# Kernel tuning notes

Hardware: AMD Instinct MI355X
Metric: run time of the kernel (lower is better)

Reference implementation:

```python
import jax, jax.numpy as jnp
import numpy as np

B = 1024
H = 2048  # hidden_size
D = 2048  # input_size

def setup_inputs() -> dict:
    key = jax.random.key(0)
    k1, k2, k3, k4 = jax.random.split(key, 4)
    x = jax.random.normal(k1, (B, D), dtype=jnp.float32)
    h = jax.random.normal(k2, (B, H), dtype=jnp.float32)
    c = jax.random.normal(k3, (B, H), dtype=jnp.float32)
    W = jax.random.normal(k4, (D + H, 4 * H), dtype=jnp.float32) * 0.02
    return {"x": x, "h": h, "c": c, "W": W}

def reference(x, h, c, W):
    # merged = cat([x, h], dim=1); weighted = merged @ W
    merged = jnp.concatenate([x, h], axis=1)          # (B, D+H)
    weighted = merged @ W                             # (B, 4H)
    hid = W.shape[1] // 4
    c_f, c_i, c_g, c_o = jnp.split(weighted, 4, axis=1)
    c_new = c * jax.nn.sigmoid(c_f) + jax.nn.sigmoid(c_i) * jnp.tanh(c_g)
    h_new = jax.nn.sigmoid(c_o) * jnp.tanh(c_new)
    return h_new
```

## Files before the change

kernel.cpp:

```cpp
#include <hip/hip_runtime.h>

typedef __attribute__((ext_vector_type(4))) float          f32x4;
typedef __attribute__((ext_vector_type(8))) __bf16         bf16x8;
typedef __attribute__((ext_vector_type(8))) unsigned short u16x8;

#define B_  1024
#define D_  2048
#define H_  2048
#define K_  4096
#define N_  8192

__device__ __forceinline__ unsigned short f2bf_rne(float f) {
  unsigned u = __builtin_bit_cast(unsigned, f);
  u += 0x7fffu + ((u >> 16) & 1u);
  return (unsigned short)(u >> 16);
}

__device__ __forceinline__ float sigf(float x) {
  return 1.f / (1.f + __expf(-x));
}
__device__ __forceinline__ float tanhf_(float x) {
  float ax = fabsf(x);
  float t  = __expf(-2.f * ax);
  float r  = (1.f - t) / (1.f + t);
  return (x < 0.f) ? -r : r;
}

typedef const __attribute__((address_space(1))) unsigned int* gptr_t;
typedef __attribute__((address_space(3))) unsigned int*       lptr_t;
__device__ __forceinline__ void gl_lds16(const void* g, void* l) {
  __builtin_amdgcn_global_load_lds((gptr_t)g, (lptr_t)l, 16, 0, 0);
}

__global__ __launch_bounds__(256) void k_convert_merged(
    const float* __restrict__ x, const float* __restrict__ h,
    unsigned short* __restrict__ merged) {
  int tid = blockIdx.x * 256 + threadIdx.x;
  int e0  = tid * 8;
  int b   = e0 >> 12;
  int col = e0 & 4095;
  const float* src = (col < D_) ? (x + (size_t)b * D_ + col)
                                : (h + (size_t)b * H_ + (col - D_));
  f32x4 v0 = *(const f32x4*)src;
  f32x4 v1 = *(const f32x4*)(src + 4);
  u16x8 o;
  o[0] = f2bf_rne(v0[0]); o[1] = f2bf_rne(v0[1]);
  o[2] = f2bf_rne(v0[2]); o[3] = f2bf_rne(v0[3]);
  o[4] = f2bf_rne(v1[0]); o[5] = f2bf_rne(v1[1]);
  o[6] = f2bf_rne(v1[2]); o[7] = f2bf_rne(v1[3]);
  *(u16x8*)(merged + e0) = o;
}

__global__ __launch_bounds__(256) void k_transpose_w(
    const float* __restrict__ W, unsigned short* __restrict__ Wt) {
  __shared__ float lt[64 * 64];
  char* lbase = (char*)lt;
  const int t   = threadIdx.x;
  const int g   = blockIdx.x & 3;
  const int jb  = blockIdx.x >> 2;
  const int n0s = g * 2048 + jb * 64;
  const int k0  = blockIdx.y * 64;
#pragma unroll
  for (int i = 0; i < 4; ++i) {
    int kk = (t >> 4) + i * 16;
    int nn = (t & 15) * 4;
    f32x4 v = *(const f32x4*)&W[(size_t)(k0 + kk) * N_ + n0s + nn];
    int by = (kk * 256 + nn * 4) ^ (((kk >> 3) & 7) << 4);
    *(f32x4*)(lbase + by) = v;
  }
  __syncthreads();
#pragma unroll
  for (int i = 0; i < 2; ++i) {
    int jl = (t >> 3) + i * 32;
    int kc = (t & 7) * 8;
    u16x8 o;
#pragma unroll
    for (int jj = 0; jj < 8; ++jj) {
      int k  = kc + jj;
      int by = (k * 256 + jl * 4) ^ (((k >> 3) & 7) << 4);
      o[jj] = f2bf_rne(*(const float*)(lbase + by));
    }
    int nrow = 4 * (jb * 64 + jl) + g;
    *(u16x8*)&Wt[(size_t)nrow * K_ + k0 + kc] = o;
  }
}

#define TM 128
#define TN 128
#define TK 64

__global__ __launch_bounds__(256) void k_gemm(
    const unsigned short* __restrict__ A,
    const unsigned short* __restrict__ Bt,
    const float* __restrict__ c,
    float* __restrict__ out) {
  __shared__ unsigned short As[TM * TK];
  __shared__ unsigned short Bs[TN * TK];
  const int t    = threadIdx.x;
  const int bx   = blockIdx.x;
  const int by   = blockIdx.y;
  const int wid  = t >> 6;
  const int lane = t & 63;
  const int wr   = wid >> 1, wc = wid & 1;
  const int ln15 = lane & 15, kq = lane >> 4;

  const int srow  = t >> 3;
  const int scolb = (t & 7) * 16;

  const char* gA = (const char*)A + (size_t)(by * TM + srow) * (K_ * 2) + scolb;
  const char* gB = (const char*)Bt + (size_t)(bx * TN + srow) * (K_ * 2) + scolb;
  char* lA = (char*)As + srow * (TK * 2) + scolb;
  char* lB = (char*)Bs + srow * (TK * 2) + scolb;

  f32x4 acc[4][4] = {};

  for (int kt = 0; kt < K_ / TK; ++kt) {
    const int gofs = kt * (TK * 2);
#pragma unroll
    for (int i = 0; i < 4; ++i) {
      gl_lds16(gA + (size_t)(i * 32) * (K_ * 2) + gofs, lA + i * 32 * (TK * 2));
      gl_lds16(gB + (size_t)(i * 32) * (K_ * 2) + gofs, lB + i * 32 * (TK * 2));
    }
    __syncthreads();
#pragma unroll
    for (int ks = 0; ks < 2; ++ks) {
      bf16x8 a[4], b[4];
#pragma unroll
      for (int mi = 0; mi < 4; ++mi)
        a[mi] = *(const bf16x8*)((const char*)As +
                 (wr * 64 + mi * 16 + ln15) * (TK * 2) + ks * 64 + kq * 16);
#pragma unroll
      for (int ni = 0; ni < 4; ++ni)
        b[ni] = *(const bf16x8*)((const char*)Bs +
                 (wc * 64 + ni * 16 + ln15) * (TK * 2) + ks * 64 + kq * 16);
#pragma unroll
      for (int mi = 0; mi < 4; ++mi)
#pragma unroll
        for (int ni = 0; ni < 4; ++ni)
          acc[mi][ni] = __builtin_amdgcn_mfma_f32_16x16x32_bf16(
              a[mi], b[ni], acc[mi][ni], 0, 0, 0);
    }
    __syncthreads();
  }

  const int crow0 = by * TM + wr * 64 + kq * 4;
  const int s     = ln15 & 3;
  const int q     = ln15 >> 2;
  const int jbase = bx * 32 + wc * 16 + q;
#pragma unroll
  for (int mi = 0; mi < 4; ++mi)
#pragma unroll
    for (int ni = 0; ni < 4; ++ni)
#pragma unroll
      for (int r = 0; r < 4; ++r) {
        float v  = acc[mi][ni][r];
        float v1 = __shfl_xor(v, 1);
        float v2 = __shfl_xor(v, 2);
        float v3 = __shfl_xor(v, 3);
        if (s == 0) {
          int row = crow0 + mi * 16 + r;
          int j   = jbase + ni * 4;
          float cv = c[(size_t)row * H_ + j];
          float cn = cv * sigf(v) + sigf(v1) * tanhf_(v2);
          out[(size_t)row * H_ + j] = sigf(v3) * tanhf_(cn);
        }
      }
}

extern "C" void kernel_launch(void* const* d_in, const int* in_sizes, int n_in,
                              void* d_out, int out_size, void* d_ws, size_t ws_size,
                              hipStream_t stream) {
  (void)in_sizes; (void)n_in; (void)out_size; (void)ws_size;
  const float* x = (const float*)d_in[0];
  const float* h = (const float*)d_in[1];
  const float* c = (const float*)d_in[2];
  const float* W = (const float*)d_in[3];
  float* out = (float*)d_out;

  char* ws = (char*)d_ws;
  unsigned short* merged = (unsigned short*)ws;
  unsigned short* Wt     = (unsigned short*)(ws + (size_t)8  * 1024 * 1024);

  k_convert_merged<<<2048, 256, 0, stream>>>(x, h, merged);
  k_transpose_w<<<dim3(128, 64), 256, 0, stream>>>(W, Wt);
  k_gemm<<<dim3(N_ / TN, B_ / TM), 256, 0, stream>>>(merged, Wt, c, out);
}
```

Measured before the change: 343.0 us.

## Interleave gate columns in 16-wide groups and use 8 waves per GEMM block

The transposed weight layout now groups the four gates in 16-column chunks rather than interleaving them per column. Each lane therefore holds all four gate values for its column in registers, and the epilogue no longer needs cross-lane shuffles or idle lanes. The GEMM block grows to 512 threads (8 waves), each computing a 32x64 sub-tile with half the accumulators. LDS loads become one contiguous 16-byte chunk per thread in two halves. The aim is to cut epilogue overhead and raise occupancy, at the cost of more waves contending for the same LDS tile and barriers.

Result: faster. 319.8 us (-6.7%).

```diff
diff --git a/kernel.cpp b/kernel.cpp
--- a/kernel.cpp
+++ b/kernel.cpp
@@ -80,7 +80,8 @@
       int by = (k * 256 + jl * 4) ^ (((k >> 3) & 7) << 4);
       o[jj] = f2bf_rne(*(const float*)(lbase + by));
     }
-    int nrow = 4 * (jb * 64 + jl) + g;
+    int j    = jb * 64 + jl;
+    int nrow = ((j >> 4) * 64) + g * 16 + (j & 15);
     *(u16x8*)&Wt[(size_t)nrow * K_ + k0 + kc] = o;
   }
 }
@@ -89,7 +90,7 @@
 #define TN 128
 #define TK 64
 
-__global__ __launch_bounds__(256) void k_gemm(
+__global__ __launch_bounds__(512, 4) void k_gemm(
     const unsigned short* __restrict__ A,
     const unsigned short* __restrict__ Bt,
     const float* __restrict__ c,
@@ -99,42 +100,42 @@
   const int t    = threadIdx.x;
   const int bx   = blockIdx.x;
   const int by   = blockIdx.y;
-  const int wid  = t >> 6;
+  const int w    = t >> 6;
   const int lane = t & 63;
-  const int wr   = wid >> 1, wc = wid & 1;
+  const int wr   = w >> 1, wc = w & 1;
   const int ln15 = lane & 15, kq = lane >> 4;
 
-  const int srow  = t >> 3;
-  const int scolb = (t & 7) * 16;
+  const int srow  = w * 8 + (lane >> 3);
+  const int chunk = (lane & 7) * 16;
 
-  const char* gA = (const char*)A + (size_t)(by * TM + srow) * (K_ * 2) + scolb;
-  const char* gB = (const char*)Bt + (size_t)(bx * TN + srow) * (K_ * 2) + scolb;
-  char* lA = (char*)As + srow * (TK * 2) + scolb;
-  char* lB = (char*)Bs + srow * (TK * 2) + scolb;
+  const char* gA = (const char*)A  + (size_t)(by * TM + srow) * (K_ * 2) + chunk;
+  const char* gB = (const char*)Bt + (size_t)(bx * TN + srow) * (K_ * 2) + chunk;
+  char* lA = (char*)As + t * 16;
+  char* lB = (char*)Bs + t * 16;
+  const size_t half = (size_t)64 * (K_ * 2);
 
-  f32x4 acc[4][4] = {};
+  f32x4 acc[2][4] = {};
 
   for (int kt = 0; kt < K_ / TK; ++kt) {
     const int gofs = kt * (TK * 2);
-#pragma unroll
-    for (int i = 0; i < 4; ++i) {
-      gl_lds16(gA + (size_t)(i * 32) * (K_ * 2) + gofs, lA + i * 32 * (TK * 2));
-      gl_lds16(gB + (size_t)(i * 32) * (K_ * 2) + gofs, lB + i * 32 * (TK * 2));
-    }
+    gl_lds16(gA + gofs,        lA);
+    gl_lds16(gA + half + gofs, lA + 8192);
+    gl_lds16(gB + gofs,        lB);
+    gl_lds16(gB + half + gofs, lB + 8192);
     __syncthreads();
 #pragma unroll
     for (int ks = 0; ks < 2; ++ks) {
-      bf16x8 a[4], b[4];
+      bf16x8 a[2], b[4];
 #pragma unroll
-      for (int mi = 0; mi < 4; ++mi)
+      for (int mi = 0; mi < 2; ++mi)
         a[mi] = *(const bf16x8*)((const char*)As +
-                 (wr * 64 + mi * 16 + ln15) * (TK * 2) + ks * 64 + kq * 16);
+                 (wr * 32 + mi * 16 + ln15) * (TK * 2) + ks * 64 + kq * 16);
 #pragma unroll
       for (int ni = 0; ni < 4; ++ni)
         b[ni] = *(const bf16x8*)((const char*)Bs +
                  (wc * 64 + ni * 16 + ln15) * (TK * 2) + ks * 64 + kq * 16);
 #pragma unroll
-      for (int mi = 0; mi < 4; ++mi)
+      for (int mi = 0; mi < 2; ++mi)
 #pragma unroll
         for (int ni = 0; ni < 4; ++ni)
           acc[mi][ni] = __builtin_amdgcn_mfma_f32_16x16x32_bf16(
@@ -143,28 +144,21 @@
     __syncthreads();
   }
 
-  const int crow0 = by * TM + wr * 64 + kq * 4;
-  const int s     = ln15 & 3;
-  const int q     = ln15 >> 2;
-  const int jbase = bx * 32 + wc * 16 + q;
+  const int row0 = by * TM + wr * 32 + kq * 4;
+  const int j    = (bx * 2 + wc) * 16 + ln15;
 #pragma unroll
-  for (int mi = 0; mi < 4; ++mi)
+  for (int mi = 0; mi < 2; ++mi)
 #pragma unroll
-    for (int ni = 0; ni < 4; ++ni)
-#pragma unroll
-      for (int r = 0; r < 4; ++r) {
-        float v  = acc[mi][ni][r];
-        float v1 = __shfl_xor(v, 1);
-        float v2 = __shfl_xor(v, 2);
-        float v3 = __shfl_xor(v, 3);
-        if (s == 0) {
-          int row = crow0 + mi * 16 + r;
-          int j   = jbase + ni * 4;
-          float cv = c[(size_t)row * H_ + j];
-          float cn = cv * sigf(v) + sigf(v1) * tanhf_(v2);
-          out[(size_t)row * H_ + j] = sigf(v3) * tanhf_(cn);
-        }
-      }
+    for (int r = 0; r < 4; ++r) {
+      int row   = row0 + mi * 16 + r;
+      float fg  = acc[mi][0][r];
+      float ig  = acc[mi][1][r];
+      float gg  = acc[mi][2][r];
+      float og  = acc[mi][3][r];
+      float cv  = c[(size_t)row * H_ + j];
+      float cn  = cv * sigf(fg) + sigf(ig) * tanhf_(gg);
+      out[(size_t)row * H_ + j] = sigf(og) * tanhf_(cn);
+    }
 }
 
 extern "C" void kernel_launch(void* const* d_in, const int* in_sizes, int n_in,
@@ -183,5 +177,5 @@
 
   k_convert_merged<<<2048, 256, 0, stream>>>(x, h, merged);
   k_transpose_w<<<dim3(128, 64), 256, 0, stream>>>(W, Wt);
-  k_gemm<<<dim3(N_ / TN, B_ / TM), 256, 0, stream>>>(merged, Wt, c, out);
+  k_gemm<<<dim3(N_ / TN, B_ / TM), 512, 0, stream>>>(merged, Wt, c, out);
 }
```
